# Kernel tuning notes

Hardware: AMD Instinct MI355X
Metric: run time of the kernel (lower is better)

## Reference

```python
import jax, jax.numpy as jnp
import numpy as np

# Model dims (match init_kwargs)
D_MODEL = 2048
N_HEADS = 16
N_GROUPS = 8
HEAD_DIM = 128
TPA_RANK = 2
TPA_Q_RANK = 6


def setup_inputs() -> dict:
    key = jax.random.key(0)
    ks = jax.random.split(key, 7)
    S, B = 4096, 2
    scale = 1.0 / np.sqrt(D_MODEL)
    inp = {
        "hidden_states": jax.random.normal(ks[0], (S, B, D_MODEL), jnp.float32),
        # weights stored [in, out] so projection is x @ W
        "W_a_q": jax.random.normal(ks[1], (D_MODEL, N_HEADS * TPA_Q_RANK), jnp.float32) * scale,
        "W_a_k": jax.random.normal(ks[2], (D_MODEL, N_GROUPS * TPA_RANK), jnp.float32) * scale,
        "W_a_v": jax.random.normal(ks[3], (D_MODEL, N_GROUPS * TPA_RANK), jnp.float32) * scale,
        "W_b_q": jax.random.normal(ks[4], (D_MODEL, TPA_Q_RANK * HEAD_DIM), jnp.float32) * scale,
        "W_b_k": jax.random.normal(ks[5], (D_MODEL, TPA_RANK * HEAD_DIM), jnp.float32) * scale,
        "W_b_v": jax.random.normal(ks[6], (D_MODEL, TPA_RANK * HEAD_DIM), jnp.float32) * scale,
    }
    return inp


def reference(hidden_states, W_a_q, W_a_k, W_a_v, W_b_q, W_b_k, W_b_v):
    S, B, _ = hidden_states.shape
    x = hidden_states
    # Six column-parallel projections (world_size=1 -> full outputs)
    a_q = (x @ W_a_q).reshape(S, B, N_HEADS, TPA_Q_RANK)
    a_k = (x @ W_a_k).reshape(S, B, N_GROUPS, TPA_RANK)
    a_v = (x @ W_a_v).reshape(S, B, N_GROUPS, TPA_RANK)
    b_q = (x @ W_b_q).reshape(S, B, TPA_Q_RANK, HEAD_DIM)
    b_k = (x @ W_b_k).reshape(S, B, TPA_RANK, HEAD_DIM)
    b_v = (x @ W_b_v).reshape(S, B, TPA_RANK, HEAD_DIM)
    # Low-rank reconstruction: per-token batched matmul over the tiny rank dim
    q = jnp.einsum('sbhr,sbrd->sbhd', a_q, b_q) / TPA_Q_RANK  # [S,B,H,D]
    k = jnp.einsum('sbgr,sbrd->sbgd', a_k, b_k) / TPA_RANK    # [S,B,G,D]
    v = jnp.einsum('sbgr,sbrd->sbgd', a_v, b_v) / TPA_RANK    # [S,B,G,D]
    heads_per_group = N_HEADS // N_GROUPS
    q = q.reshape(S, B, N_GROUPS, heads_per_group * HEAD_DIM)
    mixed_qkv = jnp.concatenate([q, k, v], axis=3).reshape(S, B, -1)
    return mixed_qkv
```

## Files before the change

### kernel.cpp

```cpp
#include <hip/hip_runtime.h>
#include <hip/hip_bf16.h>

typedef __bf16 bf16x8 __attribute__((ext_vector_type(8)));
typedef float  f32x4  __attribute__((ext_vector_type(4)));

#define GLOAD_LDS16(g, l) \
  __builtin_amdgcn_global_load_lds((const __attribute__((address_space(1))) void*)(g), \
                                   (__attribute__((address_space(3))) void*)(l), 16, 0, 0)

static __device__ __forceinline__ ushort f2bf(float f) {
  union { float f; unsigned u; } x; x.f = f;
  unsigned r = x.u + 0x7fffu + ((x.u >> 16) & 1u);
  return (ushort)(r >> 16);
}

__global__ void cast_x_k(const float4* __restrict__ in, ushort4* __restrict__ out, int n4) {
  int idx = blockIdx.x * 256 + threadIdx.x;
  int stride = gridDim.x * 256;
  for (int i = idx; i < n4; i += stride) {
    float4 v = in[i];
    ushort4 o;
    o.x = f2bf(v.x); o.y = f2bf(v.y); o.z = f2bf(v.z); o.w = f2bf(v.w);
    out[i] = o;
  }
}

__global__ void pack_wt_k(const float* __restrict__ W0, const float* __restrict__ W1,
                          const float* __restrict__ W2, const float* __restrict__ W3,
                          const float* __restrict__ W4, const float* __restrict__ W5,
                          ushort* __restrict__ Wt) {
  __shared__ ushort tile[64 * 66];
  const int k0 = blockIdx.x * 64, c0 = blockIdx.y * 64;
  const int tid = threadIdx.x;
#pragma unroll
  for (int i = 0; i < 16; ++i) {
    int idx = tid + i * 256;
    int kl = idx >> 6, cl = idx & 63;
    int c = c0 + cl, k = k0 + kl;
    const float* W; int n, lc;
    if (c < 96)       { W = W0; n = 96;  lc = c; }
    else if (c < 112) { W = W1; n = 16;  lc = c - 96; }
    else if (c < 128) { W = W2; n = 16;  lc = c - 112; }
    else if (c < 896) { W = W3; n = 768; lc = c - 128; }
    else if (c < 1152){ W = W4; n = 256; lc = c - 896; }
    else              { W = W5; n = 256; lc = c - 1152; }
    tile[cl * 66 + kl] = f2bf(W[(size_t)k * n + lc]);
  }
  __syncthreads();
#pragma unroll
  for (int i = 0; i < 16; ++i) {
    int idx = tid + i * 256;
    int cl = idx >> 6, kl = idx & 63;
    Wt[(size_t)(c0 + cl) * 2048 + (k0 + kl)] = tile[cl * 66 + kl];
  }
}

__global__ __launch_bounds__(256) void gemm_bt_k(const ushort* __restrict__ X,
                                                 const ushort* __restrict__ Wt,
                                                 float* __restrict__ Y) {
  __shared__ ushort lds[8192];
  const int tid = threadIdx.x;
  const int w = tid >> 6, lane = tid & 63;
  const int bm = blockIdx.x, bn = blockIdx.y;
  const int wr = w >> 1, wc = w & 1;

  const int s0 = w, s1 = w + 4;
  const int ra = s0 * 16 + (lane >> 2);
  const int rb = s1 * 16 + (lane >> 2);
  const int ga = (lane & 3) ^ ((ra >> 1) & 3);
  const int gb = (lane & 3) ^ ((rb >> 1) & 3);
  const ushort* gA0 = X  + (size_t)(bm * 128 + ra) * 2048 + ga * 8;
  const ushort* gA1 = X  + (size_t)(bm * 128 + rb) * 2048 + gb * 8;
  const ushort* gB0 = Wt + (size_t)(bn * 128 + ra) * 2048 + ga * 8;
  const ushort* gB1 = Wt + (size_t)(bn * 128 + rb) * 2048 + gb * 8;
  ushort* lA0 = &lds[s0 * 512];
  ushort* lA1 = &lds[s1 * 512];
  ushort* lB0 = &lds[4096 + s0 * 512];
  ushort* lB1 = &lds[4096 + s1 * 512];

  int offA[4], offB[4];
#pragma unroll
  for (int m = 0; m < 4; ++m) {
    int R = wr * 64 + m * 16 + (lane & 15);
    offA[m] = R * 32 + ((((lane >> 4) ^ ((R >> 1) & 3))) << 3);
    int C = wc * 64 + m * 16 + (lane & 15);
    offB[m] = 4096 + C * 32 + ((((lane >> 4) ^ ((C >> 1) & 3))) << 3);
  }

  f32x4 acc[4][4] = {};

  for (int kk = 0; kk < 64; ++kk) {
    const int ko = kk * 32;
    GLOAD_LDS16(gA0 + ko, lA0);
    GLOAD_LDS16(gA1 + ko, lA1);
    GLOAD_LDS16(gB0 + ko, lB0);
    GLOAD_LDS16(gB1 + ko, lB1);
    __syncthreads();

    bf16x8 a[4], b[4];
#pragma unroll
    for (int m = 0; m < 4; ++m) a[m] = *reinterpret_cast<const bf16x8*>(&lds[offA[m]]);
#pragma unroll
    for (int n = 0; n < 4; ++n) b[n] = *reinterpret_cast<const bf16x8*>(&lds[offB[n]]);
#pragma unroll
    for (int m = 0; m < 4; ++m)
#pragma unroll
      for (int n = 0; n < 4; ++n)
        acc[m][n] = __builtin_amdgcn_mfma_f32_16x16x32_bf16(a[m], b[n], acc[m][n], 0, 0, 0);

    __syncthreads();
  }

#pragma unroll
  for (int m = 0; m < 4; ++m) {
    int row0 = bm * 128 + wr * 64 + m * 16 + ((lane >> 4) << 2);
#pragma unroll
    for (int n = 0; n < 4; ++n) {
      int col = bn * 128 + wc * 64 + n * 16 + (lane & 15);
#pragma unroll
      for (int j = 0; j < 4; ++j)
        Y[(size_t)(row0 + j) * 1408 + col] = acc[m][n][j];
    }
  }
}

__global__ void recon_k(const float* __restrict__ Y, float* __restrict__ out) {
  __shared__ float L[1408];
  const int t = blockIdx.x, tid = threadIdx.x;
  const float4* src = (const float4*)(Y + (size_t)t * 1408);
  float4* Ld = (float4*)L;
  for (int i = tid; i < 352; i += 256) Ld[i] = src[i];
  __syncthreads();
  float* o = out + (size_t)t * 4096;
#pragma unroll
  for (int i = 0; i < 16; ++i) {
    int p = tid + (i << 8);
    int g = p >> 9, sub = p & 511;
    float val;
    if (sub < 256) {
      int h = (g << 1) + (sub >> 7), d = sub & 127;
      const float* a = L + h * 6;
      const float* b = L + 128 + d;
      val = (a[0] * b[0] + a[1] * b[128] + a[2] * b[256] +
             a[3] * b[384] + a[4] * b[512] + a[5] * b[640]) * (1.0f / 6.0f);
    } else if (sub < 384) {
      int d = sub - 256;
      val = 0.5f * (L[96 + (g << 1)] * L[896 + d] + L[97 + (g << 1)] * L[1024 + d]);
    } else {
      int d = sub - 384;
      val = 0.5f * (L[112 + (g << 1)] * L[1152 + d] + L[113 + (g << 1)] * L[1280 + d]);
    }
    o[p] = val;
  }
}

extern "C" void kernel_launch(void* const* d_in, const int* in_sizes, int n_in,
                              void* d_out, int out_size, void* d_ws, size_t ws_size,
                              hipStream_t stream) {
  const float* x   = (const float*)d_in[0];
  const float* Waq = (const float*)d_in[1];
  const float* Wak = (const float*)d_in[2];
  const float* Wav = (const float*)d_in[3];
  const float* Wbq = (const float*)d_in[4];
  const float* Wbk = (const float*)d_in[5];
  const float* Wbv = (const float*)d_in[6];

  ushort* Xbf = (ushort*)d_ws;
  ushort* Wt  = (ushort*)((char*)d_ws + 33554432);
  float*  Y   = (float*) ((char*)d_ws + 39321600);
  float*  out = (float*)d_out;

  cast_x_k<<<2048, 256, 0, stream>>>((const float4*)x, (ushort4*)Xbf, 16777216 / 4);
  pack_wt_k<<<dim3(32, 22), 256, 0, stream>>>(Waq, Wak, Wav, Wbq, Wbk, Wbv, Wt);
  gemm_bt_k<<<dim3(64, 11), 256, 0, stream>>>(Xbf, Wt, Y);
  recon_k<<<8192, 256, 0, stream>>>(Y, out);
}
```

Baseline: 303.0 us.

## Double-buffer GEMM LDS, remap blocks per XCD, store bf16 intermediate, vectorize recon

The GEMM now double-buffers its LDS tiles, so the global-to-LDS loads for the next K step are issued before the MFMAs on the current step, leaving one barrier per iteration. Blocks are launched as a 1D grid and remapped so that consecutive hardware-dispatched blocks (round-robin across the 8 XCDs) share A/B tiles in each XCD's L2. The intermediate projection buffer Y is stored as bf16 instead of fp32, halving its write and read traffic, at the cost of extra rounding before the reconstruction. The reconstruction kernel now writes float4 and computes four outputs per thread to cut instruction count and issue more efficient stores.

```diff
diff --git a/kernel.cpp b/kernel.cpp
--- a/kernel.cpp
+++ b/kernel.cpp
@@ -12,6 +12,10 @@
   union { float f; unsigned u; } x; x.f = f;
   unsigned r = x.u + 0x7fffu + ((x.u >> 16) & 1u);
   return (ushort)(r >> 16);
+}
+static __device__ __forceinline__ float bf2f(ushort u) {
+  union { unsigned u; float f; } x; x.u = ((unsigned)u) << 16;
+  return x.f;
 }
 
 __global__ void cast_x_k(const float4* __restrict__ in, ushort4* __restrict__ out, int n4) {
@@ -57,11 +61,13 @@
 
 __global__ __launch_bounds__(256) void gemm_bt_k(const ushort* __restrict__ X,
                                                  const ushort* __restrict__ Wt,
-                                                 float* __restrict__ Y) {
-  __shared__ ushort lds[8192];
+                                                 ushort* __restrict__ Y) {
+  __shared__ ushort lds[2][8192];
   const int tid = threadIdx.x;
   const int w = tid >> 6, lane = tid & 63;
-  const int bm = blockIdx.x, bn = blockIdx.y;
+  const int bid = blockIdx.x;
+  const int wg = (bid & 7) * 88 + (bid >> 3);
+  const int bm = wg & 63, bn = wg >> 6;
   const int wr = w >> 1, wc = w & 1;
 
   const int s0 = w, s1 = w + 4;
@@ -73,10 +79,7 @@
   const ushort* gA1 = X  + (size_t)(bm * 128 + rb) * 2048 + gb * 8;
   const ushort* gB0 = Wt + (size_t)(bn * 128 + ra) * 2048 + ga * 8;
   const ushort* gB1 = Wt + (size_t)(bn * 128 + rb) * 2048 + gb * 8;
-  ushort* lA0 = &lds[s0 * 512];
-  ushort* lA1 = &lds[s1 * 512];
-  ushort* lB0 = &lds[4096 + s0 * 512];
-  ushort* lB1 = &lds[4096 + s1 * 512];
+  const int lo0 = s0 * 512, lo1 = s1 * 512;
 
   int offA[4], offB[4];
 #pragma unroll
@@ -87,21 +90,30 @@
     offB[m] = 4096 + C * 32 + ((((lane >> 4) ^ ((C >> 1) & 3))) << 3);
   }
 
+  GLOAD_LDS16(gA0, &lds[0][lo0]);
+  GLOAD_LDS16(gA1, &lds[0][lo1]);
+  GLOAD_LDS16(gB0, &lds[0][4096 + lo0]);
+  GLOAD_LDS16(gB1, &lds[0][4096 + lo1]);
+  __syncthreads();
+
   f32x4 acc[4][4] = {};
+  int cur = 0;
 
   for (int kk = 0; kk < 64; ++kk) {
-    const int ko = kk * 32;
-    GLOAD_LDS16(gA0 + ko, lA0);
-    GLOAD_LDS16(gA1 + ko, lA1);
-    GLOAD_LDS16(gB0 + ko, lB0);
-    GLOAD_LDS16(gB1 + ko, lB1);
-    __syncthreads();
-
+    if (kk < 63) {
+      const int ko = (kk + 1) * 32;
+      ushort* nb = lds[cur ^ 1];
+      GLOAD_LDS16(gA0 + ko, nb + lo0);
+      GLOAD_LDS16(gA1 + ko, nb + lo1);
+      GLOAD_LDS16(gB0 + ko, nb + 4096 + lo0);
+      GLOAD_LDS16(gB1 + ko, nb + 4096 + lo1);
+    }
+    const ushort* cb = lds[cur];
     bf16x8 a[4], b[4];
 #pragma unroll
-    for (int m = 0; m < 4; ++m) a[m] = *reinterpret_cast<const bf16x8*>(&lds[offA[m]]);
-#pragma unroll
-    for (int n = 0; n < 4; ++n) b[n] = *reinterpret_cast<const bf16x8*>(&lds[offB[n]]);
+    for (int m = 0; m < 4; ++m) a[m] = *reinterpret_cast<const bf16x8*>(&cb[offA[m]]);
+#pragma unroll
+    for (int n = 0; n < 4; ++n) b[n] = *reinterpret_cast<const bf16x8*>(&cb[offB[n]]);
 #pragma unroll
     for (int m = 0; m < 4; ++m)
 #pragma unroll
@@ -109,6 +121,7 @@
         acc[m][n] = __builtin_amdgcn_mfma_f32_16x16x32_bf16(a[m], b[n], acc[m][n], 0, 0, 0);
 
     __syncthreads();
+    cur ^= 1;
   }
 
 #pragma unroll
@@ -119,38 +132,52 @@
       int col = bn * 128 + wc * 64 + n * 16 + (lane & 15);
 #pragma unroll
       for (int j = 0; j < 4; ++j)
-        Y[(size_t)(row0 + j) * 1408 + col] = acc[m][n][j];
+        Y[(size_t)(row0 + j) * 1408 + col] = f2bf(acc[m][n][j]);
     }
   }
 }
 
-__global__ void recon_k(const float* __restrict__ Y, float* __restrict__ out) {
+__global__ void recon_k(const ushort* __restrict__ Y, float4* __restrict__ out) {
   __shared__ float L[1408];
   const int t = blockIdx.x, tid = threadIdx.x;
-  const float4* src = (const float4*)(Y + (size_t)t * 1408);
-  float4* Ld = (float4*)L;
-  for (int i = tid; i < 352; i += 256) Ld[i] = src[i];
+  const ushort* src = Y + (size_t)t * 1408;
+  if (tid < 176) {
+    ushort4 v0 = ((const ushort4*)src)[tid * 2];
+    ushort4 v1 = ((const ushort4*)src)[tid * 2 + 1];
+    float* d = L + tid * 8;
+    d[0] = bf2f(v0.x); d[1] = bf2f(v0.y); d[2] = bf2f(v0.z); d[3] = bf2f(v0.w);
+    d[4] = bf2f(v1.x); d[5] = bf2f(v1.y); d[6] = bf2f(v1.z); d[7] = bf2f(v1.w);
+  }
   __syncthreads();
-  float* o = out + (size_t)t * 4096;
-#pragma unroll
-  for (int i = 0; i < 16; ++i) {
-    int p = tid + (i << 8);
+  float4* o = out + (size_t)t * 1024;
+#pragma unroll
+  for (int i = 0; i < 4; ++i) {
+    int q4 = tid + (i << 8);
+    int p = q4 << 2;
     int g = p >> 9, sub = p & 511;
-    float val;
+    float4 val;
     if (sub < 256) {
       int h = (g << 1) + (sub >> 7), d = sub & 127;
       const float* a = L + h * 6;
       const float* b = L + 128 + d;
-      val = (a[0] * b[0] + a[1] * b[128] + a[2] * b[256] +
-             a[3] * b[384] + a[4] * b[512] + a[5] * b[640]) * (1.0f / 6.0f);
+#pragma unroll
+      for (int c = 0; c < 4; ++c)
+        (&val.x)[c] = (a[0] * b[c] + a[1] * b[128 + c] + a[2] * b[256 + c] +
+                       a[3] * b[384 + c] + a[4] * b[512 + c] + a[5] * b[640 + c]) * (1.0f / 6.0f);
     } else if (sub < 384) {
       int d = sub - 256;
-      val = 0.5f * (L[96 + (g << 1)] * L[896 + d] + L[97 + (g << 1)] * L[1024 + d]);
+      float a0 = L[96 + (g << 1)], a1 = L[97 + (g << 1)];
+#pragma unroll
+      for (int c = 0; c < 4; ++c)
+        (&val.x)[c] = 0.5f * (a0 * L[896 + d + c] + a1 * L[1024 + d + c]);
     } else {
       int d = sub - 384;
-      val = 0.5f * (L[112 + (g << 1)] * L[1152 + d] + L[113 + (g << 1)] * L[1280 + d]);
+      float a0 = L[112 + (g << 1)], a1 = L[113 + (g << 1)];
+#pragma unroll
+      for (int c = 0; c < 4; ++c)
+        (&val.x)[c] = 0.5f * (a0 * L[1152 + d + c] + a1 * L[1280 + d + c]);
     }
-    o[p] = val;
+    o[q4] = val;
   }
 }
 
@@ -167,11 +194,11 @@
 
   ushort* Xbf = (ushort*)d_ws;
   ushort* Wt  = (ushort*)((char*)d_ws + 33554432);
-  float*  Y   = (float*) ((char*)d_ws + 39321600);
+  ushort* Y   = (ushort*)((char*)d_ws + 39321600);
   float*  out = (float*)d_out;
 
   cast_x_k<<<2048, 256, 0, stream>>>((const float4*)x, (ushort4*)Xbf, 16777216 / 4);
   pack_wt_k<<<dim3(32, 22), 256, 0, stream>>>(Waq, Wak, Wav, Wbq, Wbk, Wbv, Wt);
-  gemm_bt_k<<<dim3(64, 11), 256, 0, stream>>>(Xbf, Wt, Y);
-  recon_k<<<8192, 256, 0, stream>>>(Y, out);
-}
+  gemm_bt_k<<<704, 256, 0, stream>>>(Xbf, Wt, Y);
+  recon_k<<<8192, 256, 0, stream>>>(Y, (float4*)out);
+}
```

After: 274.2 us. 1.11x faster.
